# Kernel optimization log

Measured on AMD Instinct MI355X. Metric: run time of the kernel, lower is better.

The kernel has to match this reference:

```python
import jax, jax.numpy as jnp
import numpy as np

NUM_FREQ = 16
LIGHT_SPEED = 1.0
CLIP_VALUE = 4.0
SCALE_DIVISOR = 1024.0


def setup_inputs() -> dict:
    key = jax.random.key(0)
    k1, k2, k3, k4 = jax.random.split(key, 4)
    B, S = 4, 2048
    positions = jax.random.normal(k1, (B, S, 4), dtype=jnp.float32)
    valid_mask = jax.random.randint(k2, (B, S), 0, 2) > 0
    proj_w = jax.random.normal(k3, (1, 2 * NUM_FREQ), dtype=jnp.float32) * (1.0 / np.sqrt(2 * NUM_FREQ))
    proj_b = jax.random.normal(k4, (1,), dtype=jnp.float32) * 0.01
    return {"positions": positions, "valid_mask": valid_mask, "proj_w": proj_w, "proj_b": proj_b}


def reference(positions, valid_mask, proj_w, proj_b):
    pos = positions.astype(jnp.float32)
    # freqs = 2^0 .. 2^(num_freq-1)  (torch.logspace base 2)
    freqs = jnp.exp2(jnp.arange(NUM_FREQ, dtype=jnp.float32))
    diff = pos[:, :, None, :] - pos[:, None, :, :]            # (B,S,S,4)
    dx, dy, dz, dt = diff[..., 0], diff[..., 1], diff[..., 2], diff[..., 3]
    c_dt = LIGHT_SPEED * dt
    ds2 = c_dt * c_dt - dx * dx - dy * dy - dz * dz           # (B,S,S)
    ds = jnp.sign(ds2) * jnp.sqrt(jnp.abs(ds2) + 1e-12)
    ds = jnp.clip(ds, -CLIP_VALUE, CLIP_VALUE) / SCALE_DIVISOR
    angles = ds[..., None] * freqs                             # (B,S,S,F)
    features = jnp.concatenate([jnp.sin(angles), jnp.cos(angles)], axis=-1)  # (B,S,S,2F)
    bias = jnp.einsum('bijf,f->bij', features, proj_w[0]) + proj_b[0]
    valid_pairs = valid_mask[:, None, :] & valid_mask[:, :, None]
    bias = jnp.where(valid_pairs, bias, 0.0)
    return bias
```

## Files before the change

### kernel.cpp

```cpp
#include <hip/hip_runtime.h>
#include <hip/hip_bf16.h>

#define TABN 4096
#define NF 16

__global__ void rsb_build_table(const float* __restrict__ w,
                                const float* __restrict__ bptr,
                                float* __restrict__ tab) {
  int k = blockIdx.x * blockDim.x + threadIdx.x;
  if (k > TABN) return;
  float dsc = -4.f + 8.f * (float)k / (float)TABN;
  float x = dsc * (1.f / 1024.f);
  float acc = bptr[0];
#pragma unroll
  for (int f = 0; f < NF; ++f) {
    float a = x * (float)(1 << f);
    float s, c;
    sincosf(a, &s, &c);
    acc = fmaf(w[f], s, acc);
    acc = fmaf(w[NF + f], c, acc);
  }
  tab[k] = acc;
}

__device__ __forceinline__ float rsb_elem(const float* __restrict__ tab_s,
                                          float4 pi, float4 pj, bool valid) {
  float dx = pi.x - pj.x;
  float dy = pi.y - pj.y;
  float dz = pi.z - pj.z;
  float dt = pi.w - pj.w;
  float ds2 = __fsub_rn(
      __fsub_rn(__fsub_rn(__fmul_rn(dt, dt), __fmul_rn(dx, dx)),
                __fmul_rn(dy, dy)),
      __fmul_rn(dz, dz));
  float rr = sqrtf(fabsf(ds2) + 1e-12f);
  float dsv = (ds2 > 0.f) ? rr : ((ds2 < 0.f) ? -rr : 0.f);
  dsv = fminf(4.f, fmaxf(-4.f, dsv));
  float t = (dsv + 4.f) * (float)(TABN / 8);
  int it = (int)t;
  it = max(0, min(it, TABN - 1));
  float frac = t - (float)it;
  float v0 = tab_s[it];
  float v1 = tab_s[it + 1];
  float g = fmaf(frac, v1 - v0, v0);
  return valid ? g : 0.f;
}

__global__ __launch_bounds__(256) void rsb_main(
    const float* __restrict__ pos, const int* __restrict__ mask,
    const float* __restrict__ tab, float* __restrict__ out, int S) {
  __shared__ float4 tab4_s[TABN / 4 + 1];
  __shared__ float4 pi_s[32];
  __shared__ int mi_s[32];
  float* tab_s = (float*)tab4_s;

  const int tid = threadIdx.x;
  const int b = blockIdx.z;
  const int ibase = blockIdx.y * 32;
  const int jbase = blockIdx.x * 256;

  {
    const float4* t4 = (const float4*)tab;
#pragma unroll
    for (int r = 0; r < 4; ++r) tab4_s[r * 256 + tid] = t4[r * 256 + tid];
    if (tid == 0) tab_s[TABN] = tab[TABN];
    if (tid < 32 && (ibase + tid) < S) {
      pi_s[tid] = ((const float4*)pos)[(size_t)b * S + ibase + tid];
      mi_s[tid] = mask[(size_t)b * S + ibase + tid];
    }
  }
  __syncthreads();

  const int tx = tid & 63;
  const int ty = tid >> 6;
  const int j4 = jbase + tx * 4;
  if (j4 >= S) return;

  const float4* pjp = (const float4*)pos + (size_t)b * S + j4;
  float4 pj0 = pjp[0];
  float4 pj1 = pjp[1];
  float4 pj2 = pjp[2];
  float4 pj3 = pjp[3];
  int4 mj = *(const int4*)(mask + (size_t)b * S + j4);

#pragma unroll
  for (int r = 0; r < 8; ++r) {
    int irow = r * 4 + ty;
    int i = ibase + irow;
    if (i >= S) break;
    float4 pi = pi_s[irow];
    int mi = mi_s[irow];
    float4 o;
    o.x = rsb_elem(tab_s, pi, pj0, (mi != 0) && (mj.x != 0));
    o.y = rsb_elem(tab_s, pi, pj1, (mi != 0) && (mj.y != 0));
    o.z = rsb_elem(tab_s, pi, pj2, (mi != 0) && (mj.z != 0));
    o.w = rsb_elem(tab_s, pi, pj3, (mi != 0) && (mj.w != 0));
    *(float4*)(out + ((size_t)b * S + i) * S + j4) = o;
  }
}

extern "C" void kernel_launch(void* const* d_in, const int* in_sizes, int n_in,
                              void* d_out, int out_size, void* d_ws,
                              size_t ws_size, hipStream_t stream) {
  const float* pos = (const float*)d_in[0];
  const int* mask = (const int*)d_in[1];
  const float* w = (const float*)d_in[2];
  const float* bb = (const float*)d_in[3];
  float* out = (float*)d_out;

  const int BS = in_sizes[1];
  const int S = (int)((long long)out_size / BS);
  const int B = BS / S;

  float* tab = (float*)d_ws;

  rsb_build_table<<<(TABN + 1 + 255) / 256, 256, 0, stream>>>(w, bb, tab);

  dim3 grid((S + 255) / 256, (S + 31) / 32, B);
  rsb_main<<<grid, 256, 0, stream>>>(pos, mask, tab, out, S);
}
```

Before: 97.47 us.

## Store interpolation table as value/slope pairs and widen blocks to 512 threads

The lookup table becomes float2 pairs (value, delta), so each element does one LDS read and one FMA instead of two reads and a subtract. The sign/clamp logic uses copysign and fmed3, and the index computation collapses to a single FMA. Blocks grow to 512 threads covering 512 columns, which halves how many times the table is loaded into shared memory per output. The table builder also derives the upper frequencies with double-angle recurrences instead of calling sincos for each one, which may change accuracy slightly.

```diff
diff --git a/kernel.cpp b/kernel.cpp
--- a/kernel.cpp
+++ b/kernel.cpp
@@ -4,26 +4,45 @@
 #define TABN 4096
 #define NF 16
 
-__global__ void rsb_build_table(const float* __restrict__ w,
-                                const float* __restrict__ bptr,
-                                float* __restrict__ tab) {
-  int k = blockIdx.x * blockDim.x + threadIdx.x;
-  if (k > TABN) return;
-  float dsc = -4.f + 8.f * (float)k / (float)TABN;
-  float x = dsc * (1.f / 1024.f);
-  float acc = bptr[0];
+__device__ __forceinline__ float rsb_eval(int k, const float* __restrict__ w,
+                                          float bias) {
+  float x = (-4.f + (float)k * (1.f / 512.f)) * (1.f / 1024.f);
+  float acc = bias;
+  float s7 = 0.f, c7 = 1.f;
 #pragma unroll
-  for (int f = 0; f < NF; ++f) {
+  for (int f = 0; f < 8; ++f) {
     float a = x * (float)(1 << f);
     float s, c;
     sincosf(a, &s, &c);
     acc = fmaf(w[f], s, acc);
     acc = fmaf(w[NF + f], c, acc);
+    if (f == 7) { s7 = s; c7 = c; }
   }
-  tab[k] = acc;
+  float ss = s7, cc = c7;
+#pragma unroll
+  for (int f = 8; f < NF; ++f) {
+    float ns = 2.f * ss * cc;
+    float nc = fmaf(cc, cc, -(ss * ss));
+    ss = ns;
+    cc = nc;
+    acc = fmaf(w[f], ss, acc);
+    acc = fmaf(w[NF + f], cc, acc);
+  }
+  return acc;
 }
 
-__device__ __forceinline__ float rsb_elem(const float* __restrict__ tab_s,
+__global__ void rsb_build_table(const float* __restrict__ w,
+                                const float* __restrict__ bptr,
+                                float2* __restrict__ tab) {
+  int k = blockIdx.x * blockDim.x + threadIdx.x;
+  if (k >= TABN) return;
+  float bias = bptr[0];
+  float g0 = rsb_eval(k, w, bias);
+  float g1 = rsb_eval(k + 1, w, bias);
+  tab[k] = make_float2(g0, g1 - g0);
+}
+
+__device__ __forceinline__ float rsb_elem(const float2* __restrict__ tab_s,
                                           float4 pi, float4 pj, bool valid) {
   float dx = pi.x - pj.x;
   float dy = pi.y - pj.y;
@@ -34,36 +53,34 @@
                 __fmul_rn(dy, dy)),
       __fmul_rn(dz, dz));
   float rr = sqrtf(fabsf(ds2) + 1e-12f);
-  float dsv = (ds2 > 0.f) ? rr : ((ds2 < 0.f) ? -rr : 0.f);
-  dsv = fminf(4.f, fmaxf(-4.f, dsv));
-  float t = (dsv + 4.f) * (float)(TABN / 8);
+  float dsv = __builtin_copysignf(rr, ds2);
+  dsv = __builtin_amdgcn_fmed3f(dsv, -4.f, 4.f);
+  float t = fmaf(dsv, (float)(TABN / 8), (float)(TABN / 2));
   int it = (int)t;
-  it = max(0, min(it, TABN - 1));
+  it = min(it, TABN - 1);
   float frac = t - (float)it;
-  float v0 = tab_s[it];
-  float v1 = tab_s[it + 1];
-  float g = fmaf(frac, v1 - v0, v0);
+  float2 bs = tab_s[it];
+  float g = fmaf(frac, bs.y, bs.x);
   return valid ? g : 0.f;
 }
 
-__global__ __launch_bounds__(256) void rsb_main(
+__global__ __launch_bounds__(512, 8) void rsb_main(
     const float* __restrict__ pos, const int* __restrict__ mask,
-    const float* __restrict__ tab, float* __restrict__ out, int S) {
-  __shared__ float4 tab4_s[TABN / 4 + 1];
+    const float2* __restrict__ tab, float* __restrict__ out, int S) {
+  __shared__ float4 tab4_s[TABN / 2];
   __shared__ float4 pi_s[32];
   __shared__ int mi_s[32];
-  float* tab_s = (float*)tab4_s;
+  const float2* tab_s = (const float2*)tab4_s;
 
   const int tid = threadIdx.x;
   const int b = blockIdx.z;
   const int ibase = blockIdx.y * 32;
-  const int jbase = blockIdx.x * 256;
+  const int jbase = blockIdx.x * 512;
 
   {
     const float4* t4 = (const float4*)tab;
 #pragma unroll
-    for (int r = 0; r < 4; ++r) tab4_s[r * 256 + tid] = t4[r * 256 + tid];
-    if (tid == 0) tab_s[TABN] = tab[TABN];
+    for (int r = 0; r < 4; ++r) tab4_s[r * 512 + tid] = t4[r * 512 + tid];
     if (tid < 32 && (ibase + tid) < S) {
       pi_s[tid] = ((const float4*)pos)[(size_t)b * S + ibase + tid];
       mi_s[tid] = mask[(size_t)b * S + ibase + tid];
@@ -71,8 +88,8 @@
   }
   __syncthreads();
 
-  const int tx = tid & 63;
-  const int ty = tid >> 6;
+  const int tx = tid & 127;
+  const int ty = tid >> 7;
   const int j4 = jbase + tx * 4;
   if (j4 >= S) return;
 
@@ -89,12 +106,12 @@
     int i = ibase + irow;
     if (i >= S) break;
     float4 pi = pi_s[irow];
-    int mi = mi_s[irow];
+    bool mi = (mi_s[irow] != 0);
     float4 o;
-    o.x = rsb_elem(tab_s, pi, pj0, (mi != 0) && (mj.x != 0));
-    o.y = rsb_elem(tab_s, pi, pj1, (mi != 0) && (mj.y != 0));
-    o.z = rsb_elem(tab_s, pi, pj2, (mi != 0) && (mj.z != 0));
-    o.w = rsb_elem(tab_s, pi, pj3, (mi != 0) && (mj.w != 0));
+    o.x = rsb_elem(tab_s, pi, pj0, mi && (mj.x != 0));
+    o.y = rsb_elem(tab_s, pi, pj1, mi && (mj.y != 0));
+    o.z = rsb_elem(tab_s, pi, pj2, mi && (mj.z != 0));
+    o.w = rsb_elem(tab_s, pi, pj3, mi && (mj.w != 0));
     *(float4*)(out + ((size_t)b * S + i) * S + j4) = o;
   }
 }
@@ -112,10 +129,10 @@
   const int S = (int)((long long)out_size / BS);
   const int B = BS / S;
 
-  float* tab = (float*)d_ws;
+  float2* tab = (float2*)d_ws;
 
-  rsb_build_table<<<(TABN + 1 + 255) / 256, 256, 0, stream>>>(w, bb, tab);
+  rsb_build_table<<<(TABN + 255) / 256, 256, 0, stream>>>(w, bb, tab);
 
-  dim3 grid((S + 255) / 256, (S + 31) / 32, B);
-  rsb_main<<<grid, 256, 0, stream>>>(pos, mask, tab, out, S);
+  dim3 grid((S + 511) / 512, (S + 31) / 32, B);
+  rsb_main<<<grid, 512, 0, stream>>>(pos, mask, tab, out, S);
 }
```

New measurement: 95.43 us. -2.1%, faster.
